# Kernel tuning notes

Hardware: AMD Instinct MI355X
Metric: run time of the kernel (lower is better)

## Reference

```python
import jax, jax.numpy as jnp
import numpy as np

D_MODEL = 768
N_HEADS = 12
D_FF = 3072
EPS = 1e-6


def setup_inputs() -> dict:
    key = jax.random.key(0)
    ks = jax.random.split(key, 9)
    s = 0.02
    return {
        "x": jax.random.normal(ks[0], (2, 4096, D_MODEL), dtype=jnp.float32),
        "wq": jax.random.normal(ks[1], (D_MODEL, D_MODEL), dtype=jnp.float32) * s,
        "wk": jax.random.normal(ks[2], (D_MODEL, D_MODEL), dtype=jnp.float32) * s,
        "wv": jax.random.normal(ks[3], (D_MODEL, D_MODEL), dtype=jnp.float32) * s,
        "wo": jax.random.normal(ks[4], (D_MODEL, D_MODEL), dtype=jnp.float32) * s,
        "w1": jax.random.normal(ks[5], (D_MODEL, D_FF), dtype=jnp.float32) * s,
        "b1": jnp.zeros((D_FF,), dtype=jnp.float32),
        "w2": jax.random.normal(ks[6], (D_FF, D_MODEL), dtype=jnp.float32) * s,
        "b2": jnp.zeros((D_MODEL,), dtype=jnp.float32),
        "g1": jnp.ones((D_MODEL,), dtype=jnp.float32),
        "g2": jnp.ones((D_MODEL,), dtype=jnp.float32),
    }


def _rmsnorm(x, g):
    rms = jax.lax.rsqrt(jnp.mean(x * x, axis=-1, keepdims=True) + EPS)
    return x * rms * g


def _attn(x, wq, wk, wv, wo):
    B, T, D = x.shape
    H, Dh = N_HEADS, D // N_HEADS
    q = (x @ wq).reshape(B, T, H, Dh).transpose(0, 2, 1, 3)
    k = (x @ wk).reshape(B, T, H, Dh).transpose(0, 2, 1, 3)
    v = (x @ wv).reshape(B, T, H, Dh).transpose(0, 2, 1, 3)
    scores = jnp.einsum("bhqd,bhkd->bhqk", q, k) * (Dh ** -0.5)
    causal = jnp.triu(jnp.ones((T, T), dtype=bool), k=1)
    scores = jnp.where(causal, -jnp.inf, scores)
    attn = jax.nn.softmax(scores, axis=-1)
    out = jnp.einsum("bhqk,bhkd->bhqd", attn, v)
    out = out.transpose(0, 2, 1, 3).reshape(B, T, D)
    return out @ wo


def _ffn(x, w1, b1, w2, b2):
    h = jax.nn.gelu(x @ w1 + b1, approximate=False)
    return h @ w2 + b2


def reference(x, wq, wk, wv, wo, w1, b1, w2, b2, g1, g2):
    x = x + _attn(_rmsnorm(x, g1), wq, wk, wv, wo)
    x = x + _ffn(_rmsnorm(x, g2), w1, b1, w2, b2)
    return x
```

## Files before the change

kernel.cpp:

```cpp
#include <hip/hip_runtime.h>
#include <hip/hip_bf16.h>

typedef __attribute__((ext_vector_type(8))) short bf16x8;
typedef __attribute__((ext_vector_type(4))) short bf16x4;
typedef __attribute__((ext_vector_type(4))) float f32x4;

#define MFMA16(a, b, c) __builtin_amdgcn_mfma_f32_16x16x32_bf16((a), (b), (c), 0, 0, 0)

__device__ __forceinline__ f32x4 mfma_k16(bf16x4 a, bf16x4 b, f32x4 c) {
#if __has_builtin(__builtin_amdgcn_mfma_f32_16x16x16bf16_1k)
  return __builtin_amdgcn_mfma_f32_16x16x16bf16_1k(a, b, c, 0, 0, 0);
#elif __has_builtin(__builtin_amdgcn_mfma_f32_16x16x16_bf16)
  return __builtin_amdgcn_mfma_f32_16x16x16_bf16(a, b, c, 0, 0, 0);
#else
  asm("v_mfma_f32_16x16x16_bf16 %0, %1, %2, %0" : "+v"(c) : "v"(a), "v"(b));
  return c;
#endif
}

__device__ __forceinline__ ushort f2bf(float f) {
  union { __hip_bfloat16 h; ushort u; } cv;
  cv.h = __float2bfloat16(f);
  return cv.u;
}

__device__ __forceinline__ void gload16(const void* g, void* l) {
  __builtin_amdgcn_global_load_lds((const __attribute__((address_space(1))) void*)g,
                                   (__attribute__((address_space(3))) void*)l, 16, 0, 0);
}

__global__ void wtrans_kernel(const float* __restrict__ W, ushort* __restrict__ Wt,
                              int K, int N) {
  __shared__ float t[32][33];
  const int tx = threadIdx.x & 31, ty = threadIdx.x >> 5;
  const int nb = blockIdx.x * 32, kb = blockIdx.y * 32;
#pragma unroll
  for (int i = 0; i < 4; ++i)
    t[ty + i * 8][tx] = W[(size_t)(kb + ty + i * 8) * N + nb + tx];
  __syncthreads();
#pragma unroll
  for (int i = 0; i < 4; ++i)
    Wt[(size_t)(nb + ty + i * 8) * K + kb + tx] = f2bf(t[tx][ty + i * 8]);
}

__global__ void rmsnorm_kernel(const float* __restrict__ x, const float* __restrict__ g,
                               ushort* __restrict__ out) {
  const int row = blockIdx.x;
  const float* xr = x + (size_t)row * 768;
  const int t = threadIdx.x;
  float v0 = xr[t], v1 = xr[t + 256], v2 = xr[t + 512];
  float ss = v0 * v0 + v1 * v1 + v2 * v2;
#pragma unroll
  for (int off = 1; off < 64; off <<= 1) ss += __shfl_xor(ss, off);
  __shared__ float part[4];
  if ((t & 63) == 0) part[t >> 6] = ss;
  __syncthreads();
  const float tot = part[0] + part[1] + part[2] + part[3];
  const float r = rsqrtf(tot * (1.0f / 768.0f) + 1e-6f);
  ushort* orow = out + (size_t)row * 768;
  orow[t]       = f2bf(v0 * r * g[t]);
  orow[t + 256] = f2bf(v1 * r * g[t + 256]);
  orow[t + 512] = f2bf(v2 * r * g[t + 512]);
}

enum { EPI_BF16 = 0, EPI_VT = 1, EPI_RESID = 2, EPI_BIAS_GELU = 3, EPI_BIAS_RESID = 4 };

template <int EPI>
__global__ __launch_bounds__(256) void gemm_bt(
    const ushort* __restrict__ A, const ushort* __restrict__ Bt, void* __restrict__ Cout,
    const float* __restrict__ bias, const float* __restrict__ resid, int M, int N, int K,
    float scale) {
  __shared__ ushort As[128 * 64];
  __shared__ ushort Bs[128 * 64];
  const int tid = threadIdx.x;
  const int lane = tid & 63, wid = tid >> 6;
  const int wm = wid >> 1, wn = wid & 1;
  const int l15 = lane & 15, l4 = lane >> 4;
  const int m0 = blockIdx.y * 128, n0 = blockIdx.x * 128;
  const int srow = lane >> 3, sslot = lane & 7;
  const int skel = (sslot ^ srow) << 3;

  f32x4 acc[4][4] = {};

  for (int k0 = 0; k0 < K; k0 += 64) {
    __syncthreads();
#pragma unroll
    for (int i = 0; i < 4; ++i) {
      const int c = i * 4 + wid;
      const int row = c * 8 + srow;
      gload16(A + (size_t)(m0 + row) * K + k0 + skel, (char*)As + c * 1024);
      gload16(Bt + (size_t)(n0 + row) * K + k0 + skel, (char*)Bs + c * 1024);
    }
    __syncthreads();
#pragma unroll
    for (int ks = 0; ks < 2; ++ks) {
      bf16x8 af[4], bfr[4];
#pragma unroll
      for (int mi = 0; mi < 4; ++mi) {
        const int row = wm * 64 + mi * 16 + l15;
        const int slot = (ks * 4 + l4) ^ (row & 7);
        af[mi] = *(const bf16x8*)((const char*)As + row * 128 + slot * 16);
      }
#pragma unroll
      for (int ni = 0; ni < 4; ++ni) {
        const int row = wn * 64 + ni * 16 + l15;
        const int slot = (ks * 4 + l4) ^ (row & 7);
        bfr[ni] = *(const bf16x8*)((const char*)Bs + row * 128 + slot * 16);
      }
#pragma unroll
      for (int mi = 0; mi < 4; ++mi)
#pragma unroll
        for (int ni = 0; ni < 4; ++ni)
          acc[mi][ni] = MFMA16(af[mi], bfr[ni], acc[mi][ni]);
    }
  }

#pragma unroll
  for (int mi = 0; mi < 4; ++mi) {
#pragma unroll
    for (int ni = 0; ni < 4; ++ni) {
      const int gm = m0 + wm * 64 + mi * 16 + l4 * 4;
      const int gn = n0 + wn * 64 + ni * 16 + l15;
      f32x4 v = acc[mi][ni];
#pragma unroll
      for (int r = 0; r < 4; ++r) {
        const size_t idx = (size_t)(gm + r) * N + gn;
        const float f = v[r];
        if constexpr (EPI == EPI_BF16) {
          ((ushort*)Cout)[idx] = f2bf(f * scale);
        } else if constexpr (EPI == EPI_RESID) {
          ((float*)Cout)[idx] = f + resid[idx];
        } else if constexpr (EPI == EPI_BIAS_GELU) {
          const float u = f + bias[gn];
          const float gl = 0.5f * u * (1.0f + erff(u * 0.70710678118654752f));
          ((ushort*)Cout)[idx] = f2bf(gl);
        } else if constexpr (EPI == EPI_BIAS_RESID) {
          ((float*)Cout)[idx] = f + bias[gn] + resid[idx];
        }
      }
    }
  }
}

__global__ __launch_bounds__(256) void gemm_qkv(
    const ushort* __restrict__ A, const ushort* __restrict__ Bt,
    ushort* __restrict__ qout, ushort* __restrict__ kout, ushort* __restrict__ vtout,
    int M, int K, float qscale) {
  __shared__ ushort As[128 * 64];
  __shared__ ushort Bs[128 * 64];
  const int tid = threadIdx.x;
  const int lane = tid & 63, wid = tid >> 6;
  const int wm = wid >> 1, wn = wid & 1;
  const int l15 = lane & 15, l4 = lane >> 4;
  const int m0 = blockIdx.y * 128, n0 = blockIdx.x * 128;
  const int srow = lane >> 3, sslot = lane & 7;
  const int skel = (sslot ^ srow) << 3;

  f32x4 acc[4][4] = {};

  for (int k0 = 0; k0 < K; k0 += 64) {
    __syncthreads();
#pragma unroll
    for (int i = 0; i < 4; ++i) {
      const int c = i * 4 + wid;
      const int row = c * 8 + srow;
      gload16(A + (size_t)(m0 + row) * K + k0 + skel, (char*)As + c * 1024);
      gload16(Bt + (size_t)(n0 + row) * K + k0 + skel, (char*)Bs + c * 1024);
    }
    __syncthreads();
#pragma unroll
    for (int ks = 0; ks < 2; ++ks) {
      bf16x8 af[4], bfr[4];
#pragma unroll
      for (int mi = 0; mi < 4; ++mi) {
        const int row = wm * 64 + mi * 16 + l15;
        const int slot = (ks * 4 + l4) ^ (row & 7);
        af[mi] = *(const bf16x8*)((const char*)As + row * 128 + slot * 16);
      }
#pragma unroll
      for (int ni = 0; ni < 4; ++ni) {
        const int row = wn * 64 + ni * 16 + l15;
        const int slot = (ks * 4 + l4) ^ (row & 7);
        bfr[ni] = *(const bf16x8*)((const char*)Bs + row * 128 + slot * 16);
      }
#pragma unroll
      for (int mi = 0; mi < 4; ++mi)
#pragma unroll
        for (int ni = 0; ni < 4; ++ni)
          acc[mi][ni] = MFMA16(af[mi], bfr[ni], acc[mi][ni]);
    }
  }

  const int seg = n0 / 768;
#pragma unroll
  for (int mi = 0; mi < 4; ++mi) {
#pragma unroll
    for (int ni = 0; ni < 4; ++ni) {
      const int gm = m0 + wm * 64 + mi * 16 + l4 * 4;
      const int gn = n0 + wn * 64 + ni * 16 + l15;
      const int col = gn - seg * 768;
      f32x4 v = acc[mi][ni];
      if (seg == 0) {
#pragma unroll
        for (int r = 0; r < 4; ++r)
          qout[(size_t)(gm + r) * 768 + col] = f2bf(v[r] * qscale);
      } else if (seg == 1) {
#pragma unroll
        for (int r = 0; r < 4; ++r)
          kout[(size_t)(gm + r) * 768 + col] = f2bf(v[r]);
      } else {
        const int b = gm >> 12, tt = gm & 4095;
        const int h = col >> 6, dh = col & 63;
        ushort4 pk;
        pk.x = f2bf(v[0]); pk.y = f2bf(v[1]); pk.z = f2bf(v[2]); pk.w = f2bf(v[3]);
        *(ushort4*)(vtout + (((size_t)(b * 12 + h) * 64 + dh) * 4096 + tt)) = pk;
      }
    }
  }
}

__global__ __launch_bounds__(256, 5) void flash_attn_kernel(
    const ushort* __restrict__ Q, const ushort* __restrict__ Kb,
    const ushort* __restrict__ Vt, ushort* __restrict__ O) {
  __shared__ ushort Ks[2][64 * 64];
  __shared__ ushort Vts[2][64 * 64];
  const int tid = threadIdx.x, lane = tid & 63, wid = tid >> 6;
  const int l15 = lane & 15, l4 = lane >> 4;
  const int l7 = l15 & 7;
  const int bid = (int)blockIdx.x;
  const int idx = (bid & 7) * 192 + (bid >> 3);
  const int bh = idx >> 6, b = bh / 12, h = bh % 12;
  const int qb = 63 - (idx & 63);
  const int qbase = qb * 64;
  const int q0 = qbase + wid * 16;

  bf16x8 qf0, qf1;
  {
    const ushort* qp = Q + ((size_t)(b * 4096 + q0 + l15) * 768 + h * 64 + l4 * 8);
    qf0 = *(const bf16x8*)qp;
    qf1 = *(const bf16x8*)(qp + 32);
  }
  f32x4 oo[4] = {};
  float dsum = 0.f;

  const int srow_l = lane >> 3;
  const int sco = ((lane & 7) ^ srow_l) << 3;
  const ushort* Kbase = Kb + (size_t)b * 4096 * 768 + h * 64;
  const ushort* Vbase = Vt + (size_t)bh * 64 * 4096;
  const int c0 = wid, c1 = 4 + wid;
  const ushort* kp0 = Kbase + (size_t)(c0 * 8 + srow_l) * 768 + sco;
  const ushort* kp1 = Kbase + (size_t)(c1 * 8 + srow_l) * 768 + sco;
  const ushort* vp0 = Vbase + (size_t)(c0 * 8 + srow_l) * 4096 + sco;
  const ushort* vp1 = Vbase + (size_t)(c1 * 8 + srow_l) * 4096 + sco;
  const int nt = qb + 1;

  const int koff0 = l15 * 128 + ((l4 ^ l7) << 4);
  const int koff1 = l15 * 128 + (((4 + l4) ^ l7) << 4);
  const int vbase_off = l15 * 128 + ((l4 & 1) << 3);
  const int t2b = l4 >> 1;

  gload16(kp0, (char*)Ks + c0 * 1024);
  gload16(kp1, (char*)Ks + c1 * 1024);
  gload16(vp0, (char*)Vts + c0 * 1024);
  gload16(vp1, (char*)Vts + c1 * 1024);

  int cur = 0;
  for (int kt = 0; kt < nt; ++kt) {
    const int k0 = kt << 6;
    if (kt + 1 < nt) {
      kp0 += 64 * 768; kp1 += 64 * 768;
      vp0 += 64; vp1 += 64;
      const int nb = (cur ^ 1) * 8192;
      gload16(kp0, (char*)Ks + nb + c0 * 1024);
      gload16(kp1, (char*)Ks + nb + c1 * 1024);
      gload16(vp0, (char*)Vts + nb + c0 * 1024);
      gload16(vp1, (char*)Vts + nb + c1 * 1024);
      asm volatile("s_waitcnt vmcnt(4)" ::: "memory");
    } else {
      asm volatile("s_waitcnt vmcnt(0)" ::: "memory");
    }
    __builtin_amdgcn_s_barrier();

    const int nf = (q0 + 16 - k0) >> 4;
    const int nct = nf < 4 ? nf : 4;
    const bool has_diag = (nf <= 4);
    const char* Kc = (const char*)Ks + cur * 8192;
    const char* Vc = (const char*)Vts + cur * 8192;

    __builtin_amdgcn_s_setprio(1);
#pragma unroll
    for (int ct = 0; ct < 4; ++ct) {
      if (ct < nct) {
        f32x4 s = {0.f, 0.f, 0.f, 0.f};
        const bf16x8 kf0 = *(const bf16x8*)(Kc + ct * 2048 + koff0);
        const bf16x8 kf1 = *(const bf16x8*)(Kc + ct * 2048 + koff1);
        s = MFMA16(kf0, qf0, s);
        s = MFMA16(kf1, qf1, s);
        if (has_diag && ct == nct - 1) {
#pragma unroll
          for (int r = 0; r < 4; ++r)
            if (l4 * 4 + r > l15) s[r] = -30.f;
        }
        const float p0 = __builtin_amdgcn_exp2f(s[0]);
        const float p1 = __builtin_amdgcn_exp2f(s[1]);
        const float p2 = __builtin_amdgcn_exp2f(s[2]);
        const float p3 = __builtin_amdgcn_exp2f(s[3]);
        dsum += (p0 + p1) + (p2 + p3);
        union { bf16x4 v; ushort u[4]; } pk;
        pk.u[0] = f2bf(p0); pk.u[1] = f2bf(p1);
        pk.u[2] = f2bf(p2); pk.u[3] = f2bf(p3);
        const int xo = ((2 * ct + t2b) ^ l7) << 4;
#pragma unroll
        for (int dt = 0; dt < 4; ++dt) {
          const bf16x4 vf = *(const bf16x4*)(Vc + dt * 2048 + vbase_off + xo);
          oo[dt] = mfma_k16(pk.v, vf, oo[dt]);
        }
      }
    }
    __builtin_amdgcn_s_setprio(0);
    asm volatile("" ::: "memory");
    __builtin_amdgcn_s_barrier();
    cur ^= 1;
  }

  dsum += __shfl_xor(dsum, 16);
  dsum += __shfl_xor(dsum, 32);
  ushort* op = O + ((size_t)(b * 4096 + q0 + l4 * 4) * 768 + h * 64);
#pragma unroll
  for (int r = 0; r < 4; ++r) {
    const float inv = 1.0f / __shfl(dsum, l4 * 4 + r);
#pragma unroll
    for (int dt = 0; dt < 4; ++dt)
      op[(size_t)r * 768 + dt * 16 + l15] = f2bf(oo[dt][r] * inv);
  }
}

extern "C" void kernel_launch(void* const* d_in, const int* in_sizes, int n_in,
                              void* d_out, int out_size, void* d_ws, size_t ws_size,
                              hipStream_t stream) {
  const float* x  = (const float*)d_in[0];
  const float* wq = (const float*)d_in[1];
  const float* wk = (const float*)d_in[2];
  const float* wv = (const float*)d_in[3];
  const float* wo = (const float*)d_in[4];
  const float* w1 = (const float*)d_in[5];
  const float* b1 = (const float*)d_in[6];
  const float* w2 = (const float*)d_in[7];
  const float* b2 = (const float*)d_in[8];
  const float* g1 = (const float*)d_in[9];
  const float* g2 = (const float*)d_in[10];
  float* out = (float*)d_out;

  char* p = (char*)d_ws;
  ushort* wqT = (ushort*)p; p += (size_t)768 * 768 * 2;
  ushort* wkT = (ushort*)p; p += (size_t)768 * 768 * 2;
  ushort* wvT = (ushort*)p; p += (size_t)768 * 768 * 2;
  ushort* woT = (ushort*)p; p += (size_t)768 * 768 * 2;
  ushort* w1T = (ushort*)p; p += (size_t)3072 * 768 * 2;
  ushort* w2T = (ushort*)p; p += (size_t)768 * 3072 * 2;
  ushort* xn  = (ushort*)p; p += (size_t)8192 * 768 * 2;
  ushort* qb  = (ushort*)p; p += (size_t)8192 * 768 * 2;
  ushort* kb  = (ushort*)p; p += (size_t)8192 * 768 * 2;
  ushort* vtb = (ushort*)p; p += (size_t)8192 * 768 * 2;
  ushort* attn = (ushort*)p; p += (size_t)8192 * 768 * 2;
  float* x2 = (float*)p; p += (size_t)8192 * 768 * 4;
  ushort* hf = qb;

  const float qscale = 0.125f * 1.44269504088896340736f;

  dim3 blk(256);
  wtrans_kernel<<<dim3(24, 24), blk, 0, stream>>>(wq, wqT, 768, 768);
  wtrans_kernel<<<dim3(24, 24), blk, 0, stream>>>(wk, wkT, 768, 768);
  wtrans_kernel<<<dim3(24, 24), blk, 0, stream>>>(wv, wvT, 768, 768);
  wtrans_kernel<<<dim3(24, 24), blk, 0, stream>>>(wo, woT, 768, 768);
  wtrans_kernel<<<dim3(96, 24), blk, 0, stream>>>(w1, w1T, 768, 3072);
  wtrans_kernel<<<dim3(24, 96), blk, 0, stream>>>(w2, w2T, 3072, 768);

  rmsnorm_kernel<<<8192, blk, 0, stream>>>(x, g1, xn);

  gemm_qkv<<<dim3(18, 64), blk, 0, stream>>>(xn, wqT, qb, kb, vtb, 8192, 768, qscale);

  flash_attn_kernel<<<dim3(1536), blk, 0, stream>>>(qb, kb, vtb, attn);

  gemm_bt<EPI_RESID><<<dim3(6, 64), blk, 0, stream>>>(attn, woT, x2, nullptr, x, 8192, 768, 768, 1.0f);

  rmsnorm_kernel<<<8192, blk, 0, stream>>>(x2, g2, xn);

  gemm_bt<EPI_BIAS_GELU><<<dim3(24, 64), blk, 0, stream>>>(xn, w1T, hf, b1, nullptr, 8192, 3072, 768, 1.0f);
  gemm_bt<EPI_BIAS_RESID><<<dim3(6, 64), blk, 0, stream>>>(hf, w2T, out, b2, x2, 8192, 768, 3072, 1.0f);
}
```

Baseline: 353.7 us.

## Split flash attention KV range across two wave groups and merge weight transposes

The flash attention block grows to 512 threads: two groups of four waves each take alternating 64-key tiles of the causal KV range, with separate double-buffered LDS. Their partial outputs and row sums are reduced through shared memory before one group normalises and writes the result. This halves the serial KV loop per block to get more latency hiding and parallelism, at the cost of twice the LDS, a reduction step, and lower occupancy per block. Separately, the six weight-transpose launches are merged into one kernel to cut launch overhead.

```diff
diff --git a/kernel.cpp b/kernel.cpp
--- a/kernel.cpp
+++ b/kernel.cpp
@@ -29,11 +29,30 @@
                                    (__attribute__((address_space(3))) void*)l, 16, 0, 0);
 }
 
-__global__ void wtrans_kernel(const float* __restrict__ W, ushort* __restrict__ Wt,
-                              int K, int N) {
+__global__ void wtrans_all(const float* __restrict__ wq, const float* __restrict__ wk,
+                           const float* __restrict__ wv, const float* __restrict__ wo,
+                           const float* __restrict__ w1, const float* __restrict__ w2,
+                           ushort* __restrict__ wqT, ushort* __restrict__ wkT,
+                           ushort* __restrict__ wvT, ushort* __restrict__ woT,
+                           ushort* __restrict__ w1T, ushort* __restrict__ w2T) {
   __shared__ float t[32][33];
+  int id = blockIdx.x;
+  const float* W;
+  ushort* Wt;
+  int K, N, nbx;
+  if (id < 2304) {
+    const int m = id / 576;
+    id -= m * 576;
+    W = (m == 0) ? wq : (m == 1) ? wk : (m == 2) ? wv : wo;
+    Wt = (m == 0) ? wqT : (m == 1) ? wkT : (m == 2) ? wvT : woT;
+    K = 768; N = 768; nbx = 24;
+  } else if (id < 4608) {
+    id -= 2304; W = w1; Wt = w1T; K = 768; N = 3072; nbx = 96;
+  } else {
+    id -= 4608; W = w2; Wt = w2T; K = 3072; N = 768; nbx = 24;
+  }
+  const int nb = (id % nbx) * 32, kb = (id / nbx) * 32;
   const int tx = threadIdx.x & 31, ty = threadIdx.x >> 5;
-  const int nb = blockIdx.x * 32, kb = blockIdx.y * 32;
 #pragma unroll
   for (int i = 0; i < 4; ++i)
     t[ty + i * 8][tx] = W[(size_t)(kb + ty + i * 8) * N + nb + tx];
@@ -219,20 +238,20 @@
   }
 }
 
-__global__ __launch_bounds__(256, 5) void flash_attn_kernel(
+__global__ __launch_bounds__(512, 4) void flash_attn_kernel(
     const ushort* __restrict__ Q, const ushort* __restrict__ Kb,
     const ushort* __restrict__ Vt, ushort* __restrict__ O) {
-  __shared__ ushort Ks[2][64 * 64];
-  __shared__ ushort Vts[2][64 * 64];
+  __shared__ ushort Ks[4][64 * 64];
+  __shared__ ushort Vts[4][64 * 64];
   const int tid = threadIdx.x, lane = tid & 63, wid = tid >> 6;
-  const int l15 = lane & 15, l4 = lane >> 4;
-  const int l7 = l15 & 7;
+  const int lw = wid & 3, g = wid >> 2;
+  const int l15 = lane & 15, l4 = lane >> 4, l7 = l15 & 7;
   const int bid = (int)blockIdx.x;
   const int idx = (bid & 7) * 192 + (bid >> 3);
   const int bh = idx >> 6, b = bh / 12, h = bh % 12;
   const int qb = 63 - (idx & 63);
   const int qbase = qb * 64;
-  const int q0 = qbase + wid * 16;
+  const int q0 = qbase + lw * 16;
 
   bf16x8 qf0, qf1;
   {
@@ -247,45 +266,54 @@
   const int sco = ((lane & 7) ^ srow_l) << 3;
   const ushort* Kbase = Kb + (size_t)b * 4096 * 768 + h * 64;
   const ushort* Vbase = Vt + (size_t)bh * 64 * 4096;
-  const int c0 = wid, c1 = 4 + wid;
-  const ushort* kp0 = Kbase + (size_t)(c0 * 8 + srow_l) * 768 + sco;
-  const ushort* kp1 = Kbase + (size_t)(c1 * 8 + srow_l) * 768 + sco;
-  const ushort* vp0 = Vbase + (size_t)(c0 * 8 + srow_l) * 4096 + sco;
-  const ushort* vp1 = Vbase + (size_t)(c1 * 8 + srow_l) * 4096 + sco;
-  const int nt = qb + 1;
+  const int c0 = lw, c1 = 4 + lw;
+  const int gofs = g << 6;
+  const ushort* kp0 = Kbase + (size_t)(gofs + c0 * 8 + srow_l) * 768 + sco;
+  const ushort* kp1 = Kbase + (size_t)(gofs + c1 * 8 + srow_l) * 768 + sco;
+  const ushort* vp0 = Vbase + (size_t)(c0 * 8 + srow_l) * 4096 + gofs + sco;
+  const ushort* vp1 = Vbase + (size_t)(c1 * 8 + srow_l) * 4096 + gofs + sco;
+
+  const int nt = (qb + 2) >> 1;
+  const int qlim = qbase + 64;
 
   const int koff0 = l15 * 128 + ((l4 ^ l7) << 4);
   const int koff1 = l15 * 128 + (((4 + l4) ^ l7) << 4);
   const int vbase_off = l15 * 128 + ((l4 & 1) << 3);
   const int t2b = l4 >> 1;
 
-  gload16(kp0, (char*)Ks + c0 * 1024);
-  gload16(kp1, (char*)Ks + c1 * 1024);
-  gload16(vp0, (char*)Vts + c0 * 1024);
-  gload16(vp1, (char*)Vts + c1 * 1024);
+  char* KsB = (char*)Ks + g * 16384;
+  char* VtsB = (char*)Vts + g * 16384;
+
+  if (gofs < qlim) {
+    gload16(kp0, KsB + c0 * 1024);
+    gload16(kp1, KsB + c1 * 1024);
+    gload16(vp0, VtsB + c0 * 1024);
+    gload16(vp1, VtsB + c1 * 1024);
+  }
 
   int cur = 0;
-  for (int kt = 0; kt < nt; ++kt) {
-    const int k0 = kt << 6;
-    if (kt + 1 < nt) {
-      kp0 += 64 * 768; kp1 += 64 * 768;
-      vp0 += 64; vp1 += 64;
+  for (int j = 0; j < nt; ++j) {
+    const int k0w = (j << 7) + gofs;
+    const bool pf = (((j + 1) << 7) + gofs) < qlim;
+    if (pf) {
+      kp0 += 128 * 768; kp1 += 128 * 768;
+      vp0 += 128; vp1 += 128;
       const int nb = (cur ^ 1) * 8192;
-      gload16(kp0, (char*)Ks + nb + c0 * 1024);
-      gload16(kp1, (char*)Ks + nb + c1 * 1024);
-      gload16(vp0, (char*)Vts + nb + c0 * 1024);
-      gload16(vp1, (char*)Vts + nb + c1 * 1024);
+      gload16(kp0, KsB + nb + c0 * 1024);
+      gload16(kp1, KsB + nb + c1 * 1024);
+      gload16(vp0, VtsB + nb + c0 * 1024);
+      gload16(vp1, VtsB + nb + c1 * 1024);
       asm volatile("s_waitcnt vmcnt(4)" ::: "memory");
     } else {
       asm volatile("s_waitcnt vmcnt(0)" ::: "memory");
     }
     __builtin_amdgcn_s_barrier();
 
-    const int nf = (q0 + 16 - k0) >> 4;
-    const int nct = nf < 4 ? nf : 4;
+    const int nf = (q0 + 16 - k0w) >> 4;
+    const int nct = nf < 0 ? 0 : (nf < 4 ? nf : 4);
     const bool has_diag = (nf <= 4);
-    const char* Kc = (const char*)Ks + cur * 8192;
-    const char* Vc = (const char*)Vts + cur * 8192;
+    const char* Kc = KsB + cur * 8192;
+    const char* Vc = VtsB + cur * 8192;
 
     __builtin_amdgcn_s_setprio(1);
 #pragma unroll
@@ -323,15 +351,34 @@
     cur ^= 1;
   }
 
-  dsum += __shfl_xor(dsum, 16);
-  dsum += __shfl_xor(dsum, 32);
-  ushort* op = O + ((size_t)(b * 4096 + q0 + l4 * 4) * 768 + h * 64);
-#pragma unroll
-  for (int r = 0; r < 4; ++r) {
-    const float inv = 1.0f / __shfl(dsum, l4 * 4 + r);
+  __syncthreads();
+  float* sm = (float*)Ks;
+  if (g == 1) {
+    const int base = (lw * 64 + lane) * 17;
 #pragma unroll
     for (int dt = 0; dt < 4; ++dt)
-      op[(size_t)r * 768 + dt * 16 + l15] = f2bf(oo[dt][r] * inv);
+#pragma unroll
+      for (int r = 0; r < 4; ++r) sm[base + dt * 4 + r] = oo[dt][r];
+    sm[base + 16] = dsum;
+  }
+  __syncthreads();
+  if (g == 0) {
+    const int base = (lw * 64 + lane) * 17;
+#pragma unroll
+    for (int dt = 0; dt < 4; ++dt)
+#pragma unroll
+      for (int r = 0; r < 4; ++r) oo[dt][r] += sm[base + dt * 4 + r];
+    dsum += sm[base + 16];
+    dsum += __shfl_xor(dsum, 16);
+    dsum += __shfl_xor(dsum, 32);
+    ushort* op = O + ((size_t)(b * 4096 + q0 + l4 * 4) * 768 + h * 64);
+#pragma unroll
+    for (int r = 0; r < 4; ++r) {
+      const float inv = 1.0f / __shfl(dsum, l4 * 4 + r);
+#pragma unroll
+      for (int dt = 0; dt < 4; ++dt)
+        op[(size_t)r * 768 + dt * 16 + l15] = f2bf(oo[dt][r] * inv);
+    }
   }
 }
 
@@ -369,18 +416,14 @@
   const float qscale = 0.125f * 1.44269504088896340736f;
 
   dim3 blk(256);
-  wtrans_kernel<<<dim3(24, 24), blk, 0, stream>>>(wq, wqT, 768, 768);
-  wtrans_kernel<<<dim3(24, 24), blk, 0, stream>>>(wk, wkT, 768, 768);
-  wtrans_kernel<<<dim3(24, 24), blk, 0, stream>>>(wv, wvT, 768, 768);
-  wtrans_kernel<<<dim3(24, 24), blk, 0, stream>>>(wo, woT, 768, 768);
-  wtrans_kernel<<<dim3(96, 24), blk, 0, stream>>>(w1, w1T, 768, 3072);
-  wtrans_kernel<<<dim3(24, 96), blk, 0, stream>>>(w2, w2T, 3072, 768);
+  wtrans_all<<<dim3(6912), blk, 0, stream>>>(wq, wk, wv, wo, w1, w2,
+                                             wqT, wkT, wvT, woT, w1T, w2T);
 
   rmsnorm_kernel<<<8192, blk, 0, stream>>>(x, g1, xn);
 
   gemm_qkv<<<dim3(18, 64), blk, 0, stream>>>(xn, wqT, qb, kb, vtb, 8192, 768, qscale);
 
-  flash_attn_kernel<<<dim3(1536), blk, 0, stream>>>(qb, kb, vtb, attn);
+  flash_attn_kernel<<<dim3(1536), dim3(512), 0, stream>>>(qb, kb, vtb, attn);
 
   gemm_bt<EPI_RESID><<<dim3(6, 64), blk, 0, stream>>>(attn, woT, x2, nullptr, x, 8192, 768, 768, 1.0f);
 
```

Measured after the change: 342.6 us. 3.1% less time.

## Double-buffer GEMM LDS tiles and merge weight transposes into one launch

Applied to the files above, without the earlier changes.

Both GEMM kernels now keep two LDS buffers for the A and B tiles and prefetch the next K-slice with global_load_lds while computing on the current one. Explicit vmcnt waits and raw barriers replace the two __syncthreads per iteration. The six separate weight-transpose launches are merged into a single kernel that picks the matrix from the block index, cutting launch overhead. LDS per block doubles to 64KB, which may lower occupancy.

```diff
diff --git a/kernel.cpp b/kernel.cpp
--- a/kernel.cpp
+++ b/kernel.cpp
@@ -29,11 +29,30 @@
                                    (__attribute__((address_space(3))) void*)l, 16, 0, 0);
 }
 
-__global__ void wtrans_kernel(const float* __restrict__ W, ushort* __restrict__ Wt,
-                              int K, int N) {
+__global__ void wtrans_all(const float* __restrict__ wq, const float* __restrict__ wk,
+                           const float* __restrict__ wv, const float* __restrict__ wo,
+                           const float* __restrict__ w1, const float* __restrict__ w2,
+                           ushort* __restrict__ wqT, ushort* __restrict__ wkT,
+                           ushort* __restrict__ wvT, ushort* __restrict__ woT,
+                           ushort* __restrict__ w1T, ushort* __restrict__ w2T) {
   __shared__ float t[32][33];
+  int id = blockIdx.x;
+  const float* W;
+  ushort* Wt;
+  int K, N, nbx;
+  if (id < 2304) {
+    const int m = id / 576;
+    id -= m * 576;
+    W = (m == 0) ? wq : (m == 1) ? wk : (m == 2) ? wv : wo;
+    Wt = (m == 0) ? wqT : (m == 1) ? wkT : (m == 2) ? wvT : woT;
+    K = 768; N = 768; nbx = 24;
+  } else if (id < 4608) {
+    id -= 2304; W = w1; Wt = w1T; K = 768; N = 3072; nbx = 96;
+  } else {
+    id -= 4608; W = w2; Wt = w2T; K = 3072; N = 768; nbx = 24;
+  }
+  const int nb = (id % nbx) * 32, kb = (id / nbx) * 32;
   const int tx = threadIdx.x & 31, ty = threadIdx.x >> 5;
-  const int nb = blockIdx.x * 32, kb = blockIdx.y * 32;
 #pragma unroll
   for (int i = 0; i < 4; ++i)
     t[ty + i * 8][tx] = W[(size_t)(kb + ty + i * 8) * N + nb + tx];
@@ -70,8 +89,8 @@
     const ushort* __restrict__ A, const ushort* __restrict__ Bt, void* __restrict__ Cout,
     const float* __restrict__ bias, const float* __restrict__ resid, int M, int N, int K,
     float scale) {
-  __shared__ ushort As[128 * 64];
-  __shared__ ushort Bs[128 * 64];
+  __shared__ ushort As[2][128 * 64];
+  __shared__ ushort Bs[2][128 * 64];
   const int tid = threadIdx.x;
   const int lane = tid & 63, wid = tid >> 6;
   const int wm = wid >> 1, wn = wid & 1;
@@ -82,16 +101,34 @@
 
   f32x4 acc[4][4] = {};
 
+#pragma unroll
+  for (int i = 0; i < 4; ++i) {
+    const int c = i * 4 + wid;
+    const int row = c * 8 + srow;
+    gload16(A + (size_t)(m0 + row) * K + skel, (char*)As[0] + c * 1024);
+    gload16(Bt + (size_t)(n0 + row) * K + skel, (char*)Bs[0] + c * 1024);
+  }
+
+  int cur = 0;
   for (int k0 = 0; k0 < K; k0 += 64) {
-    __syncthreads();
-#pragma unroll
-    for (int i = 0; i < 4; ++i) {
-      const int c = i * 4 + wid;
-      const int row = c * 8 + srow;
-      gload16(A + (size_t)(m0 + row) * K + k0 + skel, (char*)As + c * 1024);
-      gload16(Bt + (size_t)(n0 + row) * K + k0 + skel, (char*)Bs + c * 1024);
-    }
-    __syncthreads();
+    if (k0 + 64 < K) {
+      char* dA = (char*)As[cur ^ 1];
+      char* dB = (char*)Bs[cur ^ 1];
+#pragma unroll
+      for (int i = 0; i < 4; ++i) {
+        const int c = i * 4 + wid;
+        const int row = c * 8 + srow;
+        gload16(A + (size_t)(m0 + row) * K + k0 + 64 + skel, dA + c * 1024);
+        gload16(Bt + (size_t)(n0 + row) * K + k0 + 64 + skel, dB + c * 1024);
+      }
+      asm volatile("s_waitcnt vmcnt(8)" ::: "memory");
+    } else {
+      asm volatile("s_waitcnt vmcnt(0)" ::: "memory");
+    }
+    __builtin_amdgcn_s_barrier();
+
+    const char* pA = (const char*)As[cur];
+    const char* pB = (const char*)Bs[cur];
 #pragma unroll
     for (int ks = 0; ks < 2; ++ks) {
       bf16x8 af[4], bfr[4];
@@ -99,13 +136,13 @@
       for (int mi = 0; mi < 4; ++mi) {
         const int row = wm * 64 + mi * 16 + l15;
         const int slot = (ks * 4 + l4) ^ (row & 7);
-        af[mi] = *(const bf16x8*)((const char*)As + row * 128 + slot * 16);
+        af[mi] = *(const bf16x8*)(pA + row * 128 + slot * 16);
       }
 #pragma unroll
       for (int ni = 0; ni < 4; ++ni) {
         const int row = wn * 64 + ni * 16 + l15;
         const int slot = (ks * 4 + l4) ^ (row & 7);
-        bfr[ni] = *(const bf16x8*)((const char*)Bs + row * 128 + slot * 16);
+        bfr[ni] = *(const bf16x8*)(pB + row * 128 + slot * 16);
       }
 #pragma unroll
       for (int mi = 0; mi < 4; ++mi)
@@ -113,6 +150,9 @@
         for (int ni = 0; ni < 4; ++ni)
           acc[mi][ni] = MFMA16(af[mi], bfr[ni], acc[mi][ni]);
     }
+    asm volatile("" ::: "memory");
+    __builtin_amdgcn_s_barrier();
+    cur ^= 1;
   }
 
 #pragma unroll
@@ -146,8 +186,8 @@
     const ushort* __restrict__ A, const ushort* __restrict__ Bt,
     ushort* __restrict__ qout, ushort* __restrict__ kout, ushort* __restrict__ vtout,
     int M, int K, float qscale) {
-  __shared__ ushort As[128 * 64];
-  __shared__ ushort Bs[128 * 64];
+  __shared__ ushort As[2][128 * 64];
+  __shared__ ushort Bs[2][128 * 64];
   const int tid = threadIdx.x;
   const int lane = tid & 63, wid = tid >> 6;
   const int wm = wid >> 1, wn = wid & 1;
@@ -158,16 +198,34 @@
 
   f32x4 acc[4][4] = {};
 
+#pragma unroll
+  for (int i = 0; i < 4; ++i) {
+    const int c = i * 4 + wid;
+    const int row = c * 8 + srow;
+    gload16(A + (size_t)(m0 + row) * K + skel, (char*)As[0] + c * 1024);
+    gload16(Bt + (size_t)(n0 + row) * K + skel, (char*)Bs[0] + c * 1024);
+  }
+
+  int cur = 0;
   for (int k0 = 0; k0 < K; k0 += 64) {
-    __syncthreads();
-#pragma unroll
-    for (int i = 0; i < 4; ++i) {
-      const int c = i * 4 + wid;
-      const int row = c * 8 + srow;
-      gload16(A + (size_t)(m0 + row) * K + k0 + skel, (char*)As + c * 1024);
-      gload16(Bt + (size_t)(n0 + row) * K + k0 + skel, (char*)Bs + c * 1024);
-    }
-    __syncthreads();
+    if (k0 + 64 < K) {
+      char* dA = (char*)As[cur ^ 1];
+      char* dB = (char*)Bs[cur ^ 1];
+#pragma unroll
+      for (int i = 0; i < 4; ++i) {
+        const int c = i * 4 + wid;
+        const int row = c * 8 + srow;
+        gload16(A + (size_t)(m0 + row) * K + k0 + 64 + skel, dA + c * 1024);
+        gload16(Bt + (size_t)(n0 + row) * K + k0 + 64 + skel, dB + c * 1024);
+      }
+      asm volatile("s_waitcnt vmcnt(8)" ::: "memory");
+    } else {
+      asm volatile("s_waitcnt vmcnt(0)" ::: "memory");
+    }
+    __builtin_amdgcn_s_barrier();
+
+    const char* pA = (const char*)As[cur];
+    const char* pB = (const char*)Bs[cur];
 #pragma unroll
     for (int ks = 0; ks < 2; ++ks) {
       bf16x8 af[4], bfr[4];
@@ -175,13 +233,13 @@
       for (int mi = 0; mi < 4; ++mi) {
         const int row = wm * 64 + mi * 16 + l15;
         const int slot = (ks * 4 + l4) ^ (row & 7);
-        af[mi] = *(const bf16x8*)((const char*)As + row * 128 + slot * 16);
+        af[mi] = *(const bf16x8*)(pA + row * 128 + slot * 16);
       }
 #pragma unroll
       for (int ni = 0; ni < 4; ++ni) {
         const int row = wn * 64 + ni * 16 + l15;
         const int slot = (ks * 4 + l4) ^ (row & 7);
-        bfr[ni] = *(const bf16x8*)((const char*)Bs + row * 128 + slot * 16);
+        bfr[ni] = *(const bf16x8*)(pB + row * 128 + slot * 16);
       }
 #pragma unroll
       for (int mi = 0; mi < 4; ++mi)
@@ -189,6 +247,9 @@
         for (int ni = 0; ni < 4; ++ni)
           acc[mi][ni] = MFMA16(af[mi], bfr[ni], acc[mi][ni]);
     }
+    asm volatile("" ::: "memory");
+    __builtin_amdgcn_s_barrier();
+    cur ^= 1;
   }
 
   const int seg = n0 / 768;
@@ -369,12 +430,8 @@
   const float qscale = 0.125f * 1.44269504088896340736f;
 
   dim3 blk(256);
-  wtrans_kernel<<<dim3(24, 24), blk, 0, stream>>>(wq, wqT, 768, 768);
-  wtrans_kernel<<<dim3(24, 24), blk, 0, stream>>>(wk, wkT, 768, 768);
-  wtrans_kernel<<<dim3(24, 24), blk, 0, stream>>>(wv, wvT, 768, 768);
-  wtrans_kernel<<<dim3(24, 24), blk, 0, stream>>>(wo, woT, 768, 768);
-  wtrans_kernel<<<dim3(96, 24), blk, 0, stream>>>(w1, w1T, 768, 3072);
-  wtrans_kernel<<<dim3(24, 96), blk, 0, stream>>>(w2, w2T, 3072, 768);
+  wtrans_all<<<dim3(6912), blk, 0, stream>>>(wq, wk, wv, wo, w1, w2,
+                                             wqT, wkT, wvT, woT, w1T, w2T);
 
   rmsnorm_kernel<<<8192, blk, 0, stream>>>(x, g1, xn);
 
```

Measured after the change: 326.9 us. 1.08x faster.
